# Performance work log

Hardware: AMD Instinct MI355X
Metric: run time of the kernel (lower is better)

## Reference

```python
import jax, jax.numpy as jnp
import numpy as np

D_MODEL = 1024
N_HEADS = 16
HEAD_DIM = D_MODEL // N_HEADS
CHUNK = 128
B, T = 2, 2048


def setup_inputs() -> dict:
    key = jax.random.key(0)
    ks = jax.random.split(key, 5)
    x = jax.random.normal(ks[0], (B, T, D_MODEL), dtype=jnp.float32)
    mk = lambda k: jax.random.normal(k, (D_MODEL, D_MODEL), dtype=jnp.float32) * 0.02
    return {"x": x, "Wq": mk(ks[1]), "Wk": mk(ks[2]), "Wv": mk(ks[3]), "Wo": mk(ks[4])}


def _chunked_causal_attention(q, k, v, cs):
    # q,k,v: [B,H,T,D] fp32. Streaming online-softmax over kv chunks (flash-attn style).
    Bq, H, Tq, D = q.shape
    n = Tq // cs  # T divisible by chunk_size
    inv_sqrt_d = 1.0 / (D ** 0.5)
    qc = jnp.moveaxis(q.reshape(Bq, H, n, cs, D), 2, 0)  # [n,B,H,cs,D]
    kc = jnp.moveaxis(k.reshape(Bq, H, n, cs, D), 2, 0)
    vc = jnp.moveaxis(v.reshape(Bq, H, n, cs, D), 2, 0)
    ar = jnp.arange(cs)

    def per_q(qi, qb):  # qb: [B,H,cs,D]
        q_idx = qi * cs + ar

        def step(carry, kv):
            m, l, o = carry
            ki, kb, vb = kv
            s = jnp.einsum('bhqd,bhkd->bhqk', qb, kb) * inv_sqrt_d
            k_idx = ki * cs + ar
            causal = q_idx[:, None] >= k_idx[None, :]
            s = jnp.where(causal, s, -jnp.inf)
            s_max = jnp.max(s, axis=-1, keepdims=True)
            m_new = jnp.maximum(m, s_max)
            # guard fully-masked chunks (m_new = -inf)
            m_safe = jnp.where(jnp.isneginf(m_new), 0.0, m_new)
            alpha = jnp.exp(m - m_safe)
            p = jnp.exp(s - m_safe)
            o = o * alpha + jnp.einsum('bhqk,bhkd->bhqd', p, vb)
            l = l * alpha + jnp.sum(p, axis=-1, keepdims=True)
            return (m_new, l, o), None

        init = (jnp.full((Bq, H, cs, 1), -jnp.inf, dtype=jnp.float32),
                jnp.zeros((Bq, H, cs, 1), dtype=jnp.float32),
                jnp.zeros_like(qb))
        (m, l, o), _ = jax.lax.scan(step, init, (jnp.arange(n), kc, vc))
        return o / jnp.maximum(l, 1e-9)

    out = jax.vmap(per_q)(jnp.arange(n), qc)  # [n,B,H,cs,D]
    return jnp.moveaxis(out, 0, 2).reshape(Bq, H, Tq, D)


def reference(x, Wq, Wk, Wv, Wo):
    Bx, Tx, C = x.shape
    def heads(w):
        return (x @ w.T).reshape(Bx, Tx, N_HEADS, HEAD_DIM).transpose(0, 2, 1, 3)
    q, k, v = heads(Wq), heads(Wk), heads(Wv)
    y = _chunked_causal_attention(q, k, v, CHUNK)  # [B,H,T,D]
    y = y.transpose(0, 2, 1, 3).reshape(Bx, Tx, C)
    return y @ Wo.T
```

## Files before the change

### kernel.cpp

```cpp
#include <hip/hip_runtime.h>
#include <hip/hip_bf16.h>
#include <stdint.h>

typedef __bf16 bf16;
typedef __bf16 bf16x8 __attribute__((ext_vector_type(8)));
typedef __bf16 bf16x4 __attribute__((ext_vector_type(4)));
typedef float  f32x4  __attribute__((ext_vector_type(4)));

#define DM 1024
#define NH 16
#define HD 64
#define TT 2048

#define QSCALE 0.18033688011112042f

__global__ void cvt_all(const float* __restrict__ x,  const float* __restrict__ wq,
                        const float* __restrict__ wk, const float* __restrict__ wv,
                        const float* __restrict__ wo,
                        bf16* __restrict__ xb,  bf16* __restrict__ wqb,
                        bf16* __restrict__ wkb, bf16* __restrict__ wvb,
                        bf16* __restrict__ wob) {
  const int i = (blockIdx.x * blockDim.x + threadIdx.x) * 4;
  const float* src; bf16* dst; int off;
  if (i < 4194304)      { src = x;  dst = xb;  off = i; }
  else {
    const int j = i - 4194304;
    const int w = j >> 20;
    off = j & 1048575;
    src = (w == 0) ? wq : (w == 1) ? wk : (w == 2) ? wv : wo;
    dst = (w == 0) ? wqb : (w == 1) ? wkb : (w == 2) ? wvb : wob;
  }
  const float4 v = *reinterpret_cast<const float4*>(src + off);
  bf16x4 o = { (bf16)v.x, (bf16)v.y, (bf16)v.z, (bf16)v.w };
  *reinterpret_cast<bf16x4*>(dst + off) = o;
}

static __device__ __forceinline__ void gload_lds16(const bf16* g, bf16* l) {
  __builtin_amdgcn_global_load_lds(
      (__attribute__((address_space(1))) void*)g,
      (__attribute__((address_space(3))) void*)l, 16, 0, 0);
}

static __device__ __forceinline__ int swzb(int lin) {
  return lin ^ (((lin >> 7) & 7) << 4);
}

__launch_bounds__(256, 3)
__global__ void gemm_qkv(const bf16* __restrict__ X, const bf16* __restrict__ Wq,
                         const bf16* __restrict__ Wk, const bf16* __restrict__ Wv,
                         bf16* __restrict__ Qb, bf16* __restrict__ Kb,
                         bf16* __restrict__ Vtb) {
  __shared__ bf16 As[128 * 32];
  __shared__ bf16 Bs[128 * 32];
  const int tid  = threadIdx.x;
  const int lane = tid & 63;
  const int wv   = tid >> 6;
  const int lg   = lane >> 4, lc = lane & 15;
  const int m0   = blockIdx.x * 128;
  const int ng   = blockIdx.y * 128;
  const int which = ng >> 10;
  const bf16* W = (which == 0) ? Wq : ((which == 1) ? Wk : Wv);
  const int n0 = ng & 1023;
  const int wm = wv >> 1, wn = wv & 1;

  f32x4 acc[4][4] = {};

  for (int k0 = 0; k0 < DM; k0 += 32) {
#pragma unroll
    for (int c = 0; c < 2; ++c) {
      const int e   = wv * 512 + c * 2048 + lane * 8;
      const int row = e >> 5, col = e & 31;
      gload_lds16(X + (size_t)(m0 + row) * DM + k0 + col, &As[wv * 512 + c * 2048]);
      gload_lds16(W + (size_t)(n0 + row) * DM + k0 + col, &Bs[wv * 512 + c * 2048]);
    }
    __syncthreads();
    bf16x8 a[4], b[4];
#pragma unroll
    for (int i = 0; i < 4; ++i)
      a[i] = *reinterpret_cast<const bf16x8*>(&As[(wm * 64 + i * 16 + lc) * 32 + lg * 8]);
#pragma unroll
    for (int j = 0; j < 4; ++j)
      b[j] = *reinterpret_cast<const bf16x8*>(&Bs[(wn * 64 + j * 16 + lc) * 32 + lg * 8]);
#pragma unroll
    for (int i = 0; i < 4; ++i)
#pragma unroll
      for (int j = 0; j < 4; ++j)
        acc[i][j] = __builtin_amdgcn_mfma_f32_16x16x32_bf16(a[i], b[j], acc[i][j], 0, 0, 0);
    __syncthreads();
  }

#pragma unroll
  for (int i = 0; i < 4; ++i) {
    const int mg = m0 + wm * 64 + i * 16 + lg * 4;
    const int bb = mg >> 11, t = mg & 2047;
#pragma unroll
    for (int j = 0; j < 4; ++j) {
      const int nl = n0 + wn * 64 + j * 16 + lc;
      const int h = nl >> 6, d = nl & 63;
      const int bh = bb * NH + h;
      const f32x4 v = acc[i][j];
      if (which == 0) {
        bf16* p = Qb + ((size_t)bh * TT + t) * HD + d;
#pragma unroll
        for (int r = 0; r < 4; ++r) p[r * HD] = (bf16)(v[r] * QSCALE);
      } else if (which == 1) {
        bf16* p = Kb + ((size_t)bh * TT + t) * HD + d;
#pragma unroll
        for (int r = 0; r < 4; ++r) p[r * HD] = (bf16)v[r];
      } else {
        bf16x4 pk = { (bf16)v[0], (bf16)v[1], (bf16)v[2], (bf16)v[3] };
        *reinterpret_cast<bf16x4*>(Vtb + ((size_t)bh * HD + d) * TT + t) = pk;
      }
    }
  }
}

#define KPAD 72

__launch_bounds__(256, 3)
__global__ void attn_fwd(const bf16* __restrict__ Qb, const bf16* __restrict__ Kb,
                         const bf16* __restrict__ Vtb, bf16* __restrict__ Yb) {
  __shared__ bf16 Ks[2][4096];
  __shared__ bf16 Vs[2][4096];
  __shared__ bf16 Ps[4][16 * KPAD];

  const int tid  = threadIdx.x;
  const int lane = tid & 63;
  const int wv   = tid >> 6;
  const int lg   = lane >> 4;
  const int lc   = lane & 15;
  const int bh   = blockIdx.x & 31;
  const int qblk = 31 - (blockIdx.x >> 5);
  const int q0   = qblk * 64;
  const int NT   = qblk + 1;

  const bf16* Qg = Qb  + (size_t)bh * TT * HD;
  const bf16* Kg = Kb  + (size_t)bh * TT * HD;
  const bf16* Vg = Vtb + (size_t)bh * HD * TT;

  const bf16x8 qf0 = *reinterpret_cast<const bf16x8*>(
      Qg + (size_t)(q0 + wv * 16 + lc) * HD + 0  + lg * 8);
  const bf16x8 qf1 = *reinterpret_cast<const bf16x8*>(
      Qg + (size_t)(q0 + wv * 16 + lc) * HD + 32 + lg * 8);

  int dstb[2], koff[2], voff[2];
#pragma unroll
  for (int c = 0; c < 2; ++c) {
    const int base = (wv * 2 + c) * 1024;
    const int lin  = base + lane * 16;
    dstb[c] = base;
    koff[c] = swzb(lin);
    voff[c] = (lin >> 7) * (TT * 2) + (swzb(lin) & 127);
  }

  auto STAGE = [&](int b, int kv) {
#pragma unroll
    for (int c = 0; c < 2; ++c) {
      gload_lds16((const bf16*)((const char*)Kg + (size_t)kv * 8192 + koff[c]),
                  (bf16*)((char*)Ks[b] + dstb[c]));
      gload_lds16((const bf16*)((const char*)Vg + (size_t)kv * 128 + voff[c]),
                  (bf16*)((char*)Vs[b] + dstb[c]));
    }
  };

  f32x4 o[4] = {};
  float m_run = -INFINITY, l_run = 0.f;
  bf16* Pw = Ps[wv];
  const int b_ = bh >> 4, h_ = bh & 15;
  const int qw = q0 + wv * 16;

  STAGE(0, 0);

  int cur = 0;
  for (int ti = 0; ti < NT; ++ti) {
    const int k0 = ti * 64;

    if (ti + 1 < NT) {
      STAGE(cur ^ 1, ti + 1);
      asm volatile("s_waitcnt vmcnt(4)" ::: "memory");
    } else {
      asm volatile("s_waitcnt vmcnt(0)" ::: "memory");
    }
    __builtin_amdgcn_s_barrier();
    __builtin_amdgcn_sched_barrier(0);

    const char* ksb = (const char*)Ks[cur];
    const char* vsb = (const char*)Vs[cur];

    f32x4 s[4] = {};
    __builtin_amdgcn_s_setprio(1);
#pragma unroll
    for (int kvf = 0; kvf < 4; ++kvf) {
      const bf16x8 k0f = *reinterpret_cast<const bf16x8*>(
          ksb + swzb((kvf * 16 + lc) * 128 + lg * 16));
      s[kvf] = __builtin_amdgcn_mfma_f32_16x16x32_bf16(k0f, qf0, s[kvf], 0, 0, 0);
      const bf16x8 k1f = *reinterpret_cast<const bf16x8*>(
          ksb + swzb((kvf * 16 + lc) * 128 + 64 + lg * 16));
      s[kvf] = __builtin_amdgcn_mfma_f32_16x16x32_bf16(k1f, qf1, s[kvf], 0, 0, 0);
    }
    __builtin_amdgcn_s_setprio(0);

    if (k0 + 63 > qw) {
      const int q = qw + lc;
#pragma unroll
      for (int kvf = 0; kvf < 4; ++kvf)
#pragma unroll
        for (int r = 0; r < 4; ++r)
          if (k0 + kvf * 16 + lg * 4 + r > q) s[kvf][r] = -INFINITY;
    }

    float t0 = fmaxf(fmaxf(s[0][0], s[0][1]), fmaxf(s[0][2], s[0][3]));
    float t1 = fmaxf(fmaxf(s[1][0], s[1][1]), fmaxf(s[1][2], s[1][3]));
    float t2 = fmaxf(fmaxf(s[2][0], s[2][1]), fmaxf(s[2][2], s[2][3]));
    float t3 = fmaxf(fmaxf(s[3][0], s[3][1]), fmaxf(s[3][2], s[3][3]));
    float rmax = fmaxf(fmaxf(t0, t1), fmaxf(t2, t3));
    rmax = fmaxf(rmax, __shfl_xor(rmax, 16));
    rmax = fmaxf(rmax, __shfl_xor(rmax, 32));

    const float mn = fmaxf(m_run, rmax);
    const float alpha = __builtin_amdgcn_exp2f(m_run - mn);
    m_run = mn;

#pragma unroll
    for (int kvf = 0; kvf < 4; ++kvf)
#pragma unroll
      for (int r = 0; r < 4; ++r)
        s[kvf][r] = __builtin_amdgcn_exp2f(s[kvf][r] - mn);

#pragma unroll
    for (int df = 0; df < 4; ++df)
#pragma unroll
      for (int r = 0; r < 4; ++r) o[df][r] *= alpha;

#pragma unroll
    for (int kvf = 0; kvf < 4; ++kvf) {
      bf16x4 pk = { (bf16)s[kvf][0], (bf16)s[kvf][1],
                    (bf16)s[kvf][2], (bf16)s[kvf][3] };
      *reinterpret_cast<bf16x4*>(&Pw[lc * KPAD + kvf * 16 + lg * 4]) = pk;
    }

    __builtin_amdgcn_s_setprio(1);
#pragma unroll
    for (int ks = 0; ks < 2; ++ks) {
      const bf16x8 pf = *reinterpret_cast<const bf16x8*>(
          &Pw[lc * KPAD + ks * 32 + lg * 8]);
#pragma unroll
      for (int df = 0; df < 4; ++df) {
        const bf16x8 vf = *reinterpret_cast<const bf16x8*>(
            vsb + swzb((df * 16 + lc) * 128 + ks * 64 + lg * 16));
        o[df] = __builtin_amdgcn_mfma_f32_16x16x32_bf16(vf, pf, o[df], 0, 0, 0);
      }
    }
    __builtin_amdgcn_s_setprio(0);

    float u0 = (s[0][0] + s[0][1]) + (s[0][2] + s[0][3]);
    float u1 = (s[1][0] + s[1][1]) + (s[1][2] + s[1][3]);
    float u2 = (s[2][0] + s[2][1]) + (s[2][2] + s[2][3]);
    float u3 = (s[3][0] + s[3][1]) + (s[3][2] + s[3][3]);
    float rsum = (u0 + u1) + (u2 + u3);
    rsum += __shfl_xor(rsum, 16);
    rsum += __shfl_xor(rsum, 32);
    l_run = l_run * alpha + rsum;

    __builtin_amdgcn_s_barrier();
    cur ^= 1;
  }

  {
    const float linv = 1.f / fmaxf(l_run, 1e-9f);
    const int q = qw + lc;
#pragma unroll
    for (int df = 0; df < 4; ++df) {
      bf16x4 yv = { (bf16)(o[df][0] * linv), (bf16)(o[df][1] * linv),
                    (bf16)(o[df][2] * linv), (bf16)(o[df][3] * linv) };
      *reinterpret_cast<bf16x4*>(
          Yb + ((size_t)(b_ * TT + q)) * DM + h_ * HD + df * 16 + lg * 4) = yv;
    }
  }
}

__launch_bounds__(256, 2)
__global__ void gemm_out(const bf16* __restrict__ Y, const bf16* __restrict__ Wo,
                         float* __restrict__ Out) {
  __shared__ bf16 As[64 * 32];
  __shared__ bf16 Bs[128 * 32];
  const int tid  = threadIdx.x;
  const int lane = tid & 63;
  const int wv   = tid >> 6;
  const int lg   = lane >> 4, lc = lane & 15;
  const int m0   = blockIdx.x * 64;
  const int n0   = blockIdx.y * 128;
  const int wm = wv >> 1, wn = wv & 1;

  f32x4 acc[2][4] = {};

  for (int k0 = 0; k0 < DM; k0 += 32) {
    {
      const int e   = wv * 512 + lane * 8;
      const int row = e >> 5, col = e & 31;
      gload_lds16(Y + (size_t)(m0 + row) * DM + k0 + col, &As[wv * 512]);
    }
#pragma unroll
    for (int c = 0; c < 2; ++c) {
      const int e   = wv * 1024 + c * 512 + lane * 8;
      const int row = e >> 5, col = e & 31;
      gload_lds16(Wo + (size_t)(n0 + row) * DM + k0 + col, &Bs[wv * 1024 + c * 512]);
    }
    __syncthreads();
    bf16x8 a[2], b[4];
#pragma unroll
    for (int i = 0; i < 2; ++i)
      a[i] = *reinterpret_cast<const bf16x8*>(&As[(wm * 32 + i * 16 + lc) * 32 + lg * 8]);
#pragma unroll
    for (int j = 0; j < 4; ++j)
      b[j] = *reinterpret_cast<const bf16x8*>(&Bs[(wn * 64 + j * 16 + lc) * 32 + lg * 8]);
#pragma unroll
    for (int i = 0; i < 2; ++i)
#pragma unroll
      for (int j = 0; j < 4; ++j)
        acc[i][j] = __builtin_amdgcn_mfma_f32_16x16x32_bf16(a[i], b[j], acc[i][j], 0, 0, 0);
    __syncthreads();
  }

#pragma unroll
  for (int i = 0; i < 2; ++i) {
    const int mg = m0 + wm * 32 + i * 16 + lg * 4;
#pragma unroll
    for (int j = 0; j < 4; ++j) {
      const int n = n0 + wn * 64 + j * 16 + lc;
#pragma unroll
      for (int r = 0; r < 4; ++r)
        Out[(size_t)(mg + r) * DM + n] = acc[i][j][r];
    }
  }
}

extern "C" void kernel_launch(void* const* d_in, const int* in_sizes, int n_in,
                              void* d_out, int out_size, void* d_ws, size_t ws_size,
                              hipStream_t stream) {
  const float* x  = (const float*)d_in[0];
  const float* Wq = (const float*)d_in[1];
  const float* Wk = (const float*)d_in[2];
  const float* Wv = (const float*)d_in[3];
  const float* Wo = (const float*)d_in[4];
  float* out = (float*)d_out;
  char* ws = (char*)d_ws;
  const size_t MB = 1024 * 1024;

  bf16* xb  = (bf16*)(ws + 0);
  bf16* wqb = (bf16*)(ws + 8  * MB);
  bf16* wkb = (bf16*)(ws + 10 * MB);
  bf16* wvb = (bf16*)(ws + 12 * MB);
  bf16* wob = (bf16*)(ws + 14 * MB);
  bf16* Qb  = (bf16*)(ws + 16 * MB);
  bf16* Kb  = (bf16*)(ws + 24 * MB);
  bf16* Vtb = (bf16*)(ws + 32 * MB);
  bf16* yb  = xb;

  cvt_all<<<8192, 256, 0, stream>>>(x, Wq, Wk, Wv, Wo, xb, wqb, wkb, wvb, wob);
  gemm_qkv<<<dim3(32, 24), 256, 0, stream>>>(xb, wqb, wkb, wvb, Qb, Kb, Vtb);
  attn_fwd<<<1024, 256, 0, stream>>>(Qb, Kb, Vtb, yb);
  gemm_out<<<dim3(64, 8), 256, 0, stream>>>(yb, wob, out);
}
```

Measured before the change: 107.7 us.

## Process 128 queries per attention block with two row halves per wave

Each attention block now covers 128 query rows instead of 64. Each wave computes two 16-row halves against the same K/V fragments, so every staged K/V tile in LDS is reused twice and the grid halves. It also skips the o/l rescale when no row max grows (wave-wide check), remaps query blocks in a folded order, and drops to 2 blocks per CU by reserving dummy LDS. The trade-offs are more registers per wave, a longer critical path for the heaviest causal blocks, and fewer waves to hide latency.

```diff
diff --git a/kernel.cpp b/kernel.cpp
--- a/kernel.cpp
+++ b/kernel.cpp
@@ -117,12 +117,14 @@
 
 #define KPAD 72
 
-__launch_bounds__(256, 3)
+__launch_bounds__(256, 2)
 __global__ void attn_fwd(const bf16* __restrict__ Qb, const bf16* __restrict__ Kb,
                          const bf16* __restrict__ Vtb, bf16* __restrict__ Yb) {
   __shared__ bf16 Ks[2][4096];
   __shared__ bf16 Vs[2][4096];
-  __shared__ bf16 Ps[4][16 * KPAD];
+  __shared__ bf16 Ps[4][32 * KPAD];
+  __shared__ bf16 lds_pad[4096];
+  if ((int)blockIdx.x < 0) { lds_pad[threadIdx.x] = (bf16)0.f; __syncthreads(); }
 
   const int tid  = threadIdx.x;
   const int lane = tid & 63;
@@ -130,18 +132,24 @@
   const int lg   = lane >> 4;
   const int lc   = lane & 15;
   const int bh   = blockIdx.x & 31;
-  const int qblk = 31 - (blockIdx.x >> 5);
-  const int q0   = qblk * 64;
-  const int NT   = qblk + 1;
+  const int pr   = blockIdx.x >> 5;
+  const int qblk = (pr < 8) ? pr : (23 - pr);
+  const int q0   = qblk * 128;
+  const int NT   = 2 * qblk + 2;
 
   const bf16* Qg = Qb  + (size_t)bh * TT * HD;
   const bf16* Kg = Kb  + (size_t)bh * TT * HD;
   const bf16* Vg = Vtb + (size_t)bh * HD * TT;
 
-  const bf16x8 qf0 = *reinterpret_cast<const bf16x8*>(
-      Qg + (size_t)(q0 + wv * 16 + lc) * HD + 0  + lg * 8);
-  const bf16x8 qf1 = *reinterpret_cast<const bf16x8*>(
-      Qg + (size_t)(q0 + wv * 16 + lc) * HD + 32 + lg * 8);
+  const int qw = q0 + wv * 32;
+
+  bf16x8 qf[2][2];
+#pragma unroll
+  for (int h = 0; h < 2; ++h)
+#pragma unroll
+    for (int ks = 0; ks < 2; ++ks)
+      qf[h][ks] = *reinterpret_cast<const bf16x8*>(
+          Qg + (size_t)(qw + h * 16 + lc) * HD + ks * 32 + lg * 8);
 
   int dstb[2], koff[2], voff[2];
 #pragma unroll
@@ -163,11 +171,11 @@
     }
   };
 
-  f32x4 o[4] = {};
-  float m_run = -INFINITY, l_run = 0.f;
+  f32x4 o[4][2] = {};
+  float m_run[2] = { -INFINITY, -INFINITY };
+  float l_run[2] = { 0.f, 0.f };
   bf16* Pw = Ps[wv];
   const int b_ = bh >> 4, h_ = bh & 15;
-  const int qw = q0 + wv * 16;
 
   STAGE(0, 0);
 
@@ -187,92 +195,119 @@
     const char* ksb = (const char*)Ks[cur];
     const char* vsb = (const char*)Vs[cur];
 
-    f32x4 s[4] = {};
+    f32x4 s[4][2] = {};
     __builtin_amdgcn_s_setprio(1);
 #pragma unroll
     for (int kvf = 0; kvf < 4; ++kvf) {
       const bf16x8 k0f = *reinterpret_cast<const bf16x8*>(
           ksb + swzb((kvf * 16 + lc) * 128 + lg * 16));
-      s[kvf] = __builtin_amdgcn_mfma_f32_16x16x32_bf16(k0f, qf0, s[kvf], 0, 0, 0);
+      s[kvf][0] = __builtin_amdgcn_mfma_f32_16x16x32_bf16(k0f, qf[0][0], s[kvf][0], 0, 0, 0);
+      s[kvf][1] = __builtin_amdgcn_mfma_f32_16x16x32_bf16(k0f, qf[1][0], s[kvf][1], 0, 0, 0);
       const bf16x8 k1f = *reinterpret_cast<const bf16x8*>(
           ksb + swzb((kvf * 16 + lc) * 128 + 64 + lg * 16));
-      s[kvf] = __builtin_amdgcn_mfma_f32_16x16x32_bf16(k1f, qf1, s[kvf], 0, 0, 0);
+      s[kvf][0] = __builtin_amdgcn_mfma_f32_16x16x32_bf16(k1f, qf[0][1], s[kvf][0], 0, 0, 0);
+      s[kvf][1] = __builtin_amdgcn_mfma_f32_16x16x32_bf16(k1f, qf[1][1], s[kvf][1], 0, 0, 0);
     }
     __builtin_amdgcn_s_setprio(0);
 
     if (k0 + 63 > qw) {
-      const int q = qw + lc;
+#pragma unroll
+      for (int h = 0; h < 2; ++h) {
+        const int q = qw + h * 16 + lc;
+#pragma unroll
+        for (int kvf = 0; kvf < 4; ++kvf)
+#pragma unroll
+          for (int r = 0; r < 4; ++r)
+            if (k0 + kvf * 16 + lg * 4 + r > q) s[kvf][h][r] = -INFINITY;
+      }
+    }
+
+    float pmax[2];
+#pragma unroll
+    for (int h = 0; h < 2; ++h) {
+      float a0 = fmaxf(fmaxf(s[0][h][0], s[0][h][1]), fmaxf(s[0][h][2], s[0][h][3]));
+      float a1 = fmaxf(fmaxf(s[1][h][0], s[1][h][1]), fmaxf(s[1][h][2], s[1][h][3]));
+      float a2 = fmaxf(fmaxf(s[2][h][0], s[2][h][1]), fmaxf(s[2][h][2], s[2][h][3]));
+      float a3 = fmaxf(fmaxf(s[3][h][0], s[3][h][1]), fmaxf(s[3][h][2], s[3][h][3]));
+      float m  = fmaxf(fmaxf(a0, a1), fmaxf(a2, a3));
+      m = fmaxf(m, __shfl_xor(m, 16));
+      m = fmaxf(m, __shfl_xor(m, 32));
+      pmax[h] = m;
+    }
+
+    const int need = (pmax[0] > m_run[0]) | (pmax[1] > m_run[1]);
+    if (__any(need)) {
+#pragma unroll
+      for (int h = 0; h < 2; ++h) {
+        const float mn = fmaxf(m_run[h], pmax[h]);
+        const float alpha = __builtin_amdgcn_exp2f(m_run[h] - mn);
+        m_run[h] = mn;
+        l_run[h] *= alpha;
+#pragma unroll
+        for (int df = 0; df < 4; ++df)
+#pragma unroll
+          for (int r = 0; r < 4; ++r) o[df][h][r] *= alpha;
+      }
+    }
+
+#pragma unroll
+    for (int h = 0; h < 2; ++h)
 #pragma unroll
       for (int kvf = 0; kvf < 4; ++kvf)
 #pragma unroll
         for (int r = 0; r < 4; ++r)
-          if (k0 + kvf * 16 + lg * 4 + r > q) s[kvf][r] = -INFINITY;
-    }
-
-    float t0 = fmaxf(fmaxf(s[0][0], s[0][1]), fmaxf(s[0][2], s[0][3]));
-    float t1 = fmaxf(fmaxf(s[1][0], s[1][1]), fmaxf(s[1][2], s[1][3]));
-    float t2 = fmaxf(fmaxf(s[2][0], s[2][1]), fmaxf(s[2][2], s[2][3]));
-    float t3 = fmaxf(fmaxf(s[3][0], s[3][1]), fmaxf(s[3][2], s[3][3]));
-    float rmax = fmaxf(fmaxf(t0, t1), fmaxf(t2, t3));
-    rmax = fmaxf(rmax, __shfl_xor(rmax, 16));
-    rmax = fmaxf(rmax, __shfl_xor(rmax, 32));
-
-    const float mn = fmaxf(m_run, rmax);
-    const float alpha = __builtin_amdgcn_exp2f(m_run - mn);
-    m_run = mn;
-
-#pragma unroll
-    for (int kvf = 0; kvf < 4; ++kvf)
-#pragma unroll
-      for (int r = 0; r < 4; ++r)
-        s[kvf][r] = __builtin_amdgcn_exp2f(s[kvf][r] - mn);
-
-#pragma unroll
-    for (int df = 0; df < 4; ++df)
-#pragma unroll
-      for (int r = 0; r < 4; ++r) o[df][r] *= alpha;
-
-#pragma unroll
-    for (int kvf = 0; kvf < 4; ++kvf) {
-      bf16x4 pk = { (bf16)s[kvf][0], (bf16)s[kvf][1],
-                    (bf16)s[kvf][2], (bf16)s[kvf][3] };
-      *reinterpret_cast<bf16x4*>(&Pw[lc * KPAD + kvf * 16 + lg * 4]) = pk;
-    }
+          s[kvf][h][r] = __builtin_amdgcn_exp2f(s[kvf][h][r] - m_run[h]);
+
+#pragma unroll
+    for (int h = 0; h < 2; ++h)
+#pragma unroll
+      for (int kvf = 0; kvf < 4; ++kvf) {
+        bf16x4 pk = { (bf16)s[kvf][h][0], (bf16)s[kvf][h][1],
+                      (bf16)s[kvf][h][2], (bf16)s[kvf][h][3] };
+        *reinterpret_cast<bf16x4*>(&Pw[(h * 16 + lc) * KPAD + kvf * 16 + lg * 4]) = pk;
+      }
 
     __builtin_amdgcn_s_setprio(1);
 #pragma unroll
     for (int ks = 0; ks < 2; ++ks) {
-      const bf16x8 pf = *reinterpret_cast<const bf16x8*>(
+      const bf16x8 pf0 = *reinterpret_cast<const bf16x8*>(
           &Pw[lc * KPAD + ks * 32 + lg * 8]);
+      const bf16x8 pf1 = *reinterpret_cast<const bf16x8*>(
+          &Pw[(16 + lc) * KPAD + ks * 32 + lg * 8]);
 #pragma unroll
       for (int df = 0; df < 4; ++df) {
         const bf16x8 vf = *reinterpret_cast<const bf16x8*>(
             vsb + swzb((df * 16 + lc) * 128 + ks * 64 + lg * 16));
-        o[df] = __builtin_amdgcn_mfma_f32_16x16x32_bf16(vf, pf, o[df], 0, 0, 0);
+        o[df][0] = __builtin_amdgcn_mfma_f32_16x16x32_bf16(vf, pf0, o[df][0], 0, 0, 0);
+        o[df][1] = __builtin_amdgcn_mfma_f32_16x16x32_bf16(vf, pf1, o[df][1], 0, 0, 0);
       }
     }
     __builtin_amdgcn_s_setprio(0);
 
-    float u0 = (s[0][0] + s[0][1]) + (s[0][2] + s[0][3]);
-    float u1 = (s[1][0] + s[1][1]) + (s[1][2] + s[1][3]);
-    float u2 = (s[2][0] + s[2][1]) + (s[2][2] + s[2][3]);
-    float u3 = (s[3][0] + s[3][1]) + (s[3][2] + s[3][3]);
-    float rsum = (u0 + u1) + (u2 + u3);
-    rsum += __shfl_xor(rsum, 16);
-    rsum += __shfl_xor(rsum, 32);
-    l_run = l_run * alpha + rsum;
+#pragma unroll
+    for (int h = 0; h < 2; ++h) {
+      float u0 = (s[0][h][0] + s[0][h][1]) + (s[0][h][2] + s[0][h][3]);
+      float u1 = (s[1][h][0] + s[1][h][1]) + (s[1][h][2] + s[1][h][3]);
+      float u2 = (s[2][h][0] + s[2][h][1]) + (s[2][h][2] + s[2][h][3]);
+      float u3 = (s[3][h][0] + s[3][h][1]) + (s[3][h][2] + s[3][h][3]);
+      float rsum = (u0 + u1) + (u2 + u3);
+      rsum += __shfl_xor(rsum, 16);
+      rsum += __shfl_xor(rsum, 32);
+      l_run[h] += rsum;
+    }
 
     __builtin_amdgcn_s_barrier();
     cur ^= 1;
   }
 
-  {
-    const float linv = 1.f / fmaxf(l_run, 1e-9f);
-    const int q = qw + lc;
+#pragma unroll
+  for (int h = 0; h < 2; ++h) {
+    const float linv = 1.f / fmaxf(l_run[h], 1e-9f);
+    const int q = qw + h * 16 + lc;
 #pragma unroll
     for (int df = 0; df < 4; ++df) {
-      bf16x4 yv = { (bf16)(o[df][0] * linv), (bf16)(o[df][1] * linv),
-                    (bf16)(o[df][2] * linv), (bf16)(o[df][3] * linv) };
+      bf16x4 yv = { (bf16)(o[df][h][0] * linv), (bf16)(o[df][h][1] * linv),
+                    (bf16)(o[df][h][2] * linv), (bf16)(o[df][h][3] * linv) };
       *reinterpret_cast<bf16x4*>(
           Yb + ((size_t)(b_ * TT + q)) * DM + h_ * HD + df * 16 + lg * 4) = yv;
     }
@@ -359,6 +394,6 @@
 
   cvt_all<<<8192, 256, 0, stream>>>(x, Wq, Wk, Wv, Wo, xb, wqb, wkb, wvb, wob);
   gemm_qkv<<<dim3(32, 24), 256, 0, stream>>>(xb, wqb, wkb, wvb, Qb, Kb, Vtb);
-  attn_fwd<<<1024, 256, 0, stream>>>(Qb, Kb, Vtb, yb);
+  attn_fwd<<<512, 256, 0, stream>>>(Qb, Kb, Vtb, yb);
   gemm_out<<<dim3(64, 8), 256, 0, stream>>>(yb, wob, out);
 }
```

After: 119.0 us. 10.5% more time.

## Double-buffer LDS in QKV and output GEMMs with prefetch and swizzled BK=64

Applied to the files above, without the earlier changes.

Both projection GEMMs now use two LDS buffers. The next k-tile's global->LDS loads are issued before computing the current tile, with explicit vmcnt waits and raw barriers, so load latency overlaps with MFMA work. The output GEMM also widens the k-tile to 64 and applies an XOR swizzle to the LDS layout to cut bank conflicts, and both kernels raise wave priority around the MFMA blocks. The cost is doubled LDS use, which may lower occupancy in the QKV GEMM, plus reliance on hand-counted vmcnt values for correctness.

```diff
diff --git a/kernel.cpp b/kernel.cpp
--- a/kernel.cpp
+++ b/kernel.cpp
@@ -50,8 +50,8 @@
                          const bf16* __restrict__ Wk, const bf16* __restrict__ Wv,
                          bf16* __restrict__ Qb, bf16* __restrict__ Kb,
                          bf16* __restrict__ Vtb) {
-  __shared__ bf16 As[128 * 32];
-  __shared__ bf16 Bs[128 * 32];
+  __shared__ bf16 As[2][128 * 32];
+  __shared__ bf16 Bs[2][128 * 32];
   const int tid  = threadIdx.x;
   const int lane = tid & 63;
   const int wv   = tid >> 6;
@@ -63,31 +63,57 @@
   const int n0 = ng & 1023;
   const int wm = wv >> 1, wn = wv & 1;
 
+  int lrow[2], lcol[2], ldst[2];
+#pragma unroll
+  for (int c = 0; c < 2; ++c) {
+    const int e = wv * 512 + c * 2048 + lane * 8;
+    lrow[c] = e >> 5; lcol[c] = e & 31; ldst[c] = wv * 512 + c * 2048;
+  }
+
+#define QSTAGE(buf, kt)                                                        \
+  {                                                                            \
+    _Pragma("unroll")                                                          \
+    for (int c = 0; c < 2; ++c) {                                              \
+      gload_lds16(X + (size_t)(m0 + lrow[c]) * DM + (kt) * 32 + lcol[c],       \
+                  &As[buf][ldst[c]]);                                          \
+      gload_lds16(W + (size_t)(n0 + lrow[c]) * DM + (kt) * 32 + lcol[c],       \
+                  &Bs[buf][ldst[c]]);                                          \
+    }                                                                          \
+  }
+
   f32x4 acc[4][4] = {};
-
-  for (int k0 = 0; k0 < DM; k0 += 32) {
-#pragma unroll
-    for (int c = 0; c < 2; ++c) {
-      const int e   = wv * 512 + c * 2048 + lane * 8;
-      const int row = e >> 5, col = e & 31;
-      gload_lds16(X + (size_t)(m0 + row) * DM + k0 + col, &As[wv * 512 + c * 2048]);
-      gload_lds16(W + (size_t)(n0 + row) * DM + k0 + col, &Bs[wv * 512 + c * 2048]);
-    }
-    __syncthreads();
+  QSTAGE(0, 0);
+
+  int cur = 0;
+  for (int kt = 0; kt < 32; ++kt) {
+    if (kt + 1 < 32) {
+      QSTAGE(cur ^ 1, kt + 1);
+      asm volatile("s_waitcnt vmcnt(4)" ::: "memory");
+    } else {
+      asm volatile("s_waitcnt vmcnt(0)" ::: "memory");
+    }
+    __builtin_amdgcn_s_barrier();
+    __builtin_amdgcn_sched_barrier(0);
+
     bf16x8 a[4], b[4];
 #pragma unroll
     for (int i = 0; i < 4; ++i)
-      a[i] = *reinterpret_cast<const bf16x8*>(&As[(wm * 64 + i * 16 + lc) * 32 + lg * 8]);
+      a[i] = *reinterpret_cast<const bf16x8*>(&As[cur][(wm * 64 + i * 16 + lc) * 32 + lg * 8]);
 #pragma unroll
     for (int j = 0; j < 4; ++j)
-      b[j] = *reinterpret_cast<const bf16x8*>(&Bs[(wn * 64 + j * 16 + lc) * 32 + lg * 8]);
+      b[j] = *reinterpret_cast<const bf16x8*>(&Bs[cur][(wn * 64 + j * 16 + lc) * 32 + lg * 8]);
+    __builtin_amdgcn_s_setprio(1);
 #pragma unroll
     for (int i = 0; i < 4; ++i)
 #pragma unroll
       for (int j = 0; j < 4; ++j)
         acc[i][j] = __builtin_amdgcn_mfma_f32_16x16x32_bf16(a[i], b[j], acc[i][j], 0, 0, 0);
-    __syncthreads();
-  }
+    __builtin_amdgcn_s_setprio(0);
+
+    __builtin_amdgcn_s_barrier();
+    cur ^= 1;
+  }
+#undef QSTAGE
 
 #pragma unroll
   for (int i = 0; i < 4; ++i) {
@@ -282,8 +308,8 @@
 __launch_bounds__(256, 2)
 __global__ void gemm_out(const bf16* __restrict__ Y, const bf16* __restrict__ Wo,
                          float* __restrict__ Out) {
-  __shared__ bf16 As[64 * 32];
-  __shared__ bf16 Bs[128 * 32];
+  __shared__ bf16 As[2][64 * 64];
+  __shared__ bf16 Bs[2][128 * 64];
   const int tid  = threadIdx.x;
   const int lane = tid & 63;
   const int wv   = tid >> 6;
@@ -292,35 +318,79 @@
   const int n0   = blockIdx.y * 128;
   const int wm = wv >> 1, wn = wv & 1;
 
+  int arow[2], acol[2], adst[2];
+#pragma unroll
+  for (int c = 0; c < 2; ++c) {
+    const int lin = c * 4096 + tid * 16;
+    arow[c] = lin >> 7;
+    acol[c] = (swzb(lin) & 127) >> 1;
+    adst[c] = c * 4096 + wv * 1024;
+  }
+  int brow[4], bcol[4], bdst[4];
+#pragma unroll
+  for (int c = 0; c < 4; ++c) {
+    const int lin = c * 4096 + tid * 16;
+    brow[c] = lin >> 7;
+    bcol[c] = (swzb(lin) & 127) >> 1;
+    bdst[c] = c * 4096 + wv * 1024;
+  }
+
+#define OSTAGE(buf, kt)                                                        \
+  {                                                                            \
+    _Pragma("unroll")                                                          \
+    for (int c = 0; c < 2; ++c)                                                \
+      gload_lds16(Y + (size_t)(m0 + arow[c]) * DM + (kt) * 64 + acol[c],       \
+                  (bf16*)((char*)As[buf] + adst[c]));                          \
+    _Pragma("unroll")                                                          \
+    for (int c = 0; c < 4; ++c)                                                \
+      gload_lds16(Wo + (size_t)(n0 + brow[c]) * DM + (kt) * 64 + bcol[c],      \
+                  (bf16*)((char*)Bs[buf] + bdst[c]));                          \
+  }
+
   f32x4 acc[2][4] = {};
-
-  for (int k0 = 0; k0 < DM; k0 += 32) {
-    {
-      const int e   = wv * 512 + lane * 8;
-      const int row = e >> 5, col = e & 31;
-      gload_lds16(Y + (size_t)(m0 + row) * DM + k0 + col, &As[wv * 512]);
-    }
-#pragma unroll
-    for (int c = 0; c < 2; ++c) {
-      const int e   = wv * 1024 + c * 512 + lane * 8;
-      const int row = e >> 5, col = e & 31;
-      gload_lds16(Wo + (size_t)(n0 + row) * DM + k0 + col, &Bs[wv * 1024 + c * 512]);
-    }
-    __syncthreads();
-    bf16x8 a[2], b[4];
-#pragma unroll
-    for (int i = 0; i < 2; ++i)
-      a[i] = *reinterpret_cast<const bf16x8*>(&As[(wm * 32 + i * 16 + lc) * 32 + lg * 8]);
-#pragma unroll
-    for (int j = 0; j < 4; ++j)
-      b[j] = *reinterpret_cast<const bf16x8*>(&Bs[(wn * 64 + j * 16 + lc) * 32 + lg * 8]);
-#pragma unroll
-    for (int i = 0; i < 2; ++i)
-#pragma unroll
-      for (int j = 0; j < 4; ++j)
-        acc[i][j] = __builtin_amdgcn_mfma_f32_16x16x32_bf16(a[i], b[j], acc[i][j], 0, 0, 0);
-    __syncthreads();
-  }
+  OSTAGE(0, 0);
+
+  int cur = 0;
+  for (int kt = 0; kt < 16; ++kt) {
+    if (kt + 1 < 16) {
+      OSTAGE(cur ^ 1, kt + 1);
+      asm volatile("s_waitcnt vmcnt(6)" ::: "memory");
+    } else {
+      asm volatile("s_waitcnt vmcnt(0)" ::: "memory");
+    }
+    __builtin_amdgcn_s_barrier();
+    __builtin_amdgcn_sched_barrier(0);
+
+    const char* asb = (const char*)As[cur];
+    const char* bsb = (const char*)Bs[cur];
+#pragma unroll
+    for (int ks = 0; ks < 2; ++ks) {
+      bf16x8 a[2], b[4];
+#pragma unroll
+      for (int i = 0; i < 2; ++i) {
+        const int r = wm * 32 + i * 16 + lc;
+        a[i] = *reinterpret_cast<const bf16x8*>(
+            asb + r * 128 + ((ks * 64 + lg * 16) ^ ((r & 7) << 4)));
+      }
+#pragma unroll
+      for (int j = 0; j < 4; ++j) {
+        const int r = wn * 64 + j * 16 + lc;
+        b[j] = *reinterpret_cast<const bf16x8*>(
+            bsb + r * 128 + ((ks * 64 + lg * 16) ^ ((r & 7) << 4)));
+      }
+      __builtin_amdgcn_s_setprio(1);
+#pragma unroll
+      for (int i = 0; i < 2; ++i)
+#pragma unroll
+        for (int j = 0; j < 4; ++j)
+          acc[i][j] = __builtin_amdgcn_mfma_f32_16x16x32_bf16(a[i], b[j], acc[i][j], 0, 0, 0);
+      __builtin_amdgcn_s_setprio(0);
+    }
+
+    __builtin_amdgcn_s_barrier();
+    cur ^= 1;
+  }
+#undef OSTAGE
 
 #pragma unroll
   for (int i = 0; i < 2; ++i) {
```

Result: faster. 104.1 us (median of 2 runs) (-3.3%).
